# Optimization experiments

Measured on AMD Instinct MI355X. Metric: run time of the kernel, lower is better.

The kernel has to match this reference:

```python
import jax, jax.numpy as jnp
import numpy as np

N = 1024  # batch rows; each row has 480 features

def setup_inputs() -> dict:
    key = jax.random.key(0)
    kx, kS, kT, kH, kL = jax.random.split(key, 5)
    x = jax.random.normal(kx, (N, 480), dtype=jnp.float32)
    S = jax.random.normal(kS, (30, 2, 15), dtype=jnp.float32)    # buffer
    T = jax.random.normal(kT, (30, 15), dtype=jnp.float32)       # param
    H = jax.random.normal(kH, (45, 4096), dtype=jnp.float32)     # buffer (hash matrix)
    LUT = jax.random.normal(kL, (10, 4096, 2), dtype=jnp.float32)  # param (codebook)
    return {"x": x, "S": S, "T": T, "H": H, "LUT": LUT}

def reference(x, S, T, H, LUT):
    # (N, 480) -> (N, 8, 30, 2)
    x4 = x.reshape(-1, 8, 30, 2)
    # project each 2-vector through S: (N, 8, 30, 15)
    y = jnp.einsum('abcd,cdk->abck', x4, S) - T - 1e-4
    # straight-through sign-tanh binarization
    tanh = jnp.tanh(y)
    y = jax.lax.stop_gradient(jnp.sign(y) - tanh) + tanh
    # (N, 8, 10, 45): 30*15 = 10*(3*15)
    y = y.reshape(-1, 8, 10, 45)
    # hash scores over 4096 codes: (N, 8, 10, 4096)
    scores = jnp.einsum('bpcd,dk->bpck', y, H)
    idx = jnp.argmax(scores, axis=-1)  # (N, 8, 10) int
    # one_hot @ LUT is exactly a gather: out[b,p,c,:] = LUT[c, idx[b,p,c], :]
    out = LUT[jnp.arange(10)[None, None, :], idx]  # (N, 8, 10, 2)
    return out
```

## Files before the change

### kernel.cpp

```cpp
#include <hip/hip_runtime.h>
#include <math.h>

#define M_ROWS  81920
#define NCOLS   4096
#define KPAD    48
#define NCHUNK  4
#define CHUNKC  (NCOLS / NCHUNK)
#define CROUNDS (CHUNKC / 32)
#define GHALVES 3072
#define LO_SCALE 4096.0f
#define INV_LO   (1.0f / 4096.0f)

typedef _Float16 f16x8  __attribute__((ext_vector_type(8)));
typedef float    f32x16 __attribute__((ext_vector_type(16)));


__global__ void build_B_kernel(const float* __restrict__ H,
                               _Float16* __restrict__ Bfrag) {
    const int n = blockIdx.x * 256 + threadIdx.x;
    _Float16 hi[KPAD], lo[KPAD];
    #pragma unroll
    for (int k = 0; k < 45; ++k) {
        const float h = H[k * NCOLS + n];
        const _Float16 h1 = (_Float16)h;
        hi[k] = h1;
        lo[k] = (_Float16)((h - (float)h1) * LO_SCALE);
    }
    #pragma unroll
    for (int k = 45; k < KPAD; ++k) { hi[k] = (_Float16)0.f; lo[k] = (_Float16)0.f; }

    const int g = n >> 5;
    const int c = n & 31;
    _Float16* gbase = Bfrag + (size_t)g * GHALVES;
    #pragma unroll
    for (int f = 0; f < 6; ++f) {
        const int kt = (f < 3) ? f : f - 3;
        const _Float16* src = ((f < 3) ? hi : lo) + kt * 16;
        #pragma unroll
        for (int h = 0; h < 2; ++h) {
            *(f16x8*)(gbase + f * 512 + (h * 32 + c) * 8) =
                *(const f16x8*)(src + h * 8);
        }
    }
}

__global__ __launch_bounds__(512, 2) void score_argmax_kernel(
        const float* __restrict__ x,
        const float* __restrict__ S,
        const float* __restrict__ T,
        const _Float16* __restrict__ Bfrag,
        const float* __restrict__ LUT,
        float* __restrict__ out) {
    const int tid  = threadIdx.x;
    const int lane = tid & 63;
    const int l31  = lane & 31;
    const int half = lane >> 5;
    const int wid   = tid >> 6;
    const int chunk = wid & 3;
    const int rtile = wid >> 2;
    const int rowblk = blockIdx.x * 64;
    const int rowbase = rowblk + rtile * 32;

    __shared__ float lds_best[NCHUNK][64];
    __shared__ int   lds_bidx[NCHUNK][64];

    f16x8 afr[3];
    {
        const int row  = rowbase + l31;
        const int pair = row / 10;
        const int c2   = row - pair * 10;
        const int a    = pair >> 3;
        const int b    = pair & 7;
        const float* xp = x + a * 480 + b * 60;
        #pragma unroll
        for (int kt = 0; kt < 3; ++kt) {
            #pragma unroll
            for (int j = 0; j < 8; ++j) {
                const int k    = kt * 16 + half * 8 + j;
                const bool pad = (k >= 45);
                const int kcl  = pad ? 0 : k;
                const int cc   = kcl / 15;
                const int kk   = kcl - cc * 15;
                const int c    = c2 * 3 + cc;
                const float x0 = xp[c * 2 + 0];
                const float x1 = xp[c * 2 + 1];
                float v = x0 * S[(c * 2 + 0) * 15 + kk] + x1 * S[(c * 2 + 1) * 15 + kk];
                v = v - T[c * 15 + kk] - 1e-4f;
                const float yv = (v > 0.f) ? 1.f : ((v < 0.f) ? -1.f : 0.f);
                afr[kt][j] = pad ? (_Float16)0.f : (_Float16)yv;
            }
        }
    }

    float best[16];
    int   bidx[16];
    #pragma unroll
    for (int e = 0; e < 16; ++e) { best[e] = -INFINITY; bidx[e] = 0; }

    const int colbase0 = chunk * CHUNKC;
    const int gbase0   = colbase0 >> 5;
    const _Float16* lanep = Bfrag + (size_t)lane * 8;

#define PREFETCH(dst, rr) do {                                              \
        const _Float16* fp_ = lanep + (size_t)(gbase0 + (rr)) * GHALVES;    \
        _Pragma("unroll")                                                   \
        for (int f_ = 0; f_ < 6; ++f_)                                      \
            (dst)[f_] = *(const f16x8*)(fp_ + f_ * 512);                    \
    } while (0)

#define COMPUTE(buf, ct) do {                                               \
        f32x16 ch = {0.f};                                                  \
        f32x16 cl = {0.f};                                                  \
        ch = __builtin_amdgcn_mfma_f32_32x32x16_f16(afr[0], (buf)[0], ch, 0, 0, 0); \
        ch = __builtin_amdgcn_mfma_f32_32x32x16_f16(afr[1], (buf)[1], ch, 0, 0, 0); \
        ch = __builtin_amdgcn_mfma_f32_32x32x16_f16(afr[2], (buf)[2], ch, 0, 0, 0); \
        cl = __builtin_amdgcn_mfma_f32_32x32x16_f16(afr[0], (buf)[3], cl, 0, 0, 0); \
        cl = __builtin_amdgcn_mfma_f32_32x32x16_f16(afr[1], (buf)[4], cl, 0, 0, 0); \
        cl = __builtin_amdgcn_mfma_f32_32x32x16_f16(afr[2], (buf)[5], cl, 0, 0, 0); \
        const int mycol_ = colbase0 + (ct) * 32 + l31;                      \
        _Pragma("unroll")                                                   \
        for (int e_ = 0; e_ < 16; ++e_) {                                   \
            const float s_ = fmaf(cl[e_], INV_LO, ch[e_]);                  \
            if (s_ > best[e_]) bidx[e_] = mycol_;          \
            best[e_] = fmaxf(best[e_], s_);                                 \
        }                                                                   \
    } while (0)

    f16x8 cb[6], nb[6];
    PREFETCH(cb, 0);
    for (int it = 0; it < CROUNDS; it += 2) {
        PREFETCH(nb, it + 1);
        COMPUTE(cb, it);
        PREFETCH(cb, (it + 2) & 31);
        COMPUTE(nb, it + 1);
    }
#undef PREFETCH
#undef COMPUTE

    #pragma unroll
    for (int m = 1; m < 32; m <<= 1) {
        #pragma unroll
        for (int e = 0; e < 16; ++e) {
            const float ov = __shfl_xor(best[e], m, 64);
            const int   oi = __shfl_xor(bidx[e], m, 64);
            if (ov > best[e] || (ov == best[e] && oi < bidx[e])) {
                best[e] = ov; bidx[e] = oi;
            }
        }
    }

    if (l31 == 0) {
        #pragma unroll
        for (int e = 0; e < 16; ++e) {
            const int r64 = rtile * 32 + (e & 3) + 8 * (e >> 2) + 4 * half;
            lds_best[chunk][r64] = best[e];
            lds_bidx[chunk][r64] = bidx[e];
        }
    }
    __syncthreads();

    if (tid < 64) {
        const int row = rowblk + tid;
        float bv = lds_best[0][tid];
        int   bi = lds_bidx[0][tid];
        #pragma unroll
        for (int c = 1; c < NCHUNK; ++c) {
            const float v = lds_best[c][tid];
            const int   i = lds_bidx[c][tid];
            if (v > bv) { bv = v; bi = i; }
        }
        const int pair = row / 10;
        const int c2   = row - pair * 10;
        const float* l = LUT + ((size_t)c2 * NCOLS + bi) * 2;
        out[row * 2 + 0] = l[0];
        out[row * 2 + 1] = l[1];
    }
}

extern "C" void kernel_launch(void* const* d_in, const int* in_sizes, int n_in,
                              void* d_out, int out_size, void* d_ws, size_t ws_size,
                              hipStream_t stream) {
    const float* x   = (const float*)d_in[0];
    const float* S   = (const float*)d_in[1];
    const float* T   = (const float*)d_in[2];
    const float* H   = (const float*)d_in[3];
    const float* LUT = (const float*)d_in[4];
    float* out = (float*)d_out;

    _Float16* Bfrag = (_Float16*)d_ws;

    build_B_kernel<<<16, 256, 0, stream>>>(H, Bfrag);
    score_argmax_kernel<<<1280, 512, 0, stream>>>(x, S, T, Bfrag, LUT, out);
}
```

Before: 181.0 us.

## Split column chunks across blocks and merge argmax via 64-bit atomicMax

Each block now handles 256 rows for a single column chunk (8 waves, one row tile each) instead of 64 rows across 4 chunks. The cross-chunk argmax merge moves from a shared-memory reduction to a global atomicMax on a packed key (order-preserving float bits, inverted index for lowest-index ties), and a separate kernel then does the LUT gather. The intent is to drop the block-wide barrier and LDS step and to change how blocks share B-fragment loads. In exchange it adds global atomics, an extra kernel launch, and zeroing of the key buffer.

```diff
diff --git a/kernel.cpp b/kernel.cpp
--- a/kernel.cpp
+++ b/kernel.cpp
@@ -16,7 +16,8 @@
 
 
 __global__ void build_B_kernel(const float* __restrict__ H,
-                               _Float16* __restrict__ Bfrag) {
+                               _Float16* __restrict__ Bfrag,
+                               unsigned long long* __restrict__ keys) {
     const int n = blockIdx.x * 256 + threadIdx.x;
     _Float16 hi[KPAD], lo[KPAD];
     #pragma unroll
@@ -42,6 +43,8 @@
                 *(const f16x8*)(src + h * 8);
         }
     }
+    #pragma unroll
+    for (int i = 0; i < 20; ++i) keys[(size_t)n * 20 + i] = 0ull;
 }
 
 __global__ __launch_bounds__(512, 2) void score_argmax_kernel(
@@ -49,20 +52,15 @@
         const float* __restrict__ S,
         const float* __restrict__ T,
         const _Float16* __restrict__ Bfrag,
-        const float* __restrict__ LUT,
-        float* __restrict__ out) {
+        unsigned long long* __restrict__ keys) {
     const int tid  = threadIdx.x;
     const int lane = tid & 63;
     const int l31  = lane & 31;
     const int half = lane >> 5;
-    const int wid   = tid >> 6;
-    const int chunk = wid & 3;
-    const int rtile = wid >> 2;
-    const int rowblk = blockIdx.x * 64;
-    const int rowbase = rowblk + rtile * 32;
-
-    __shared__ float lds_best[NCHUNK][64];
-    __shared__ int   lds_bidx[NCHUNK][64];
+    const int wid  = tid >> 6;
+    const int chunk  = blockIdx.x / 320;
+    const int rowblk = (blockIdx.x - chunk * 320) * 256;
+    const int rowbase = rowblk + wid * 32;
 
     f16x8 afr[3];
     {
@@ -152,29 +150,28 @@
     if (l31 == 0) {
         #pragma unroll
         for (int e = 0; e < 16; ++e) {
-            const int r64 = rtile * 32 + (e & 3) + 8 * (e >> 2) + 4 * half;
-            lds_best[chunk][r64] = best[e];
-            lds_bidx[chunk][r64] = bidx[e];
+            const int row = rowbase + (e & 3) + 8 * (e >> 2) + 4 * half;
+            const unsigned u = __float_as_uint(best[e]);
+            const unsigned mono = (u & 0x80000000u) ? ~u : (u | 0x80000000u);
+            const unsigned long long key =
+                ((unsigned long long)mono << 32) | (unsigned)(4095 - bidx[e]);
+            atomicMax(&keys[row], key);
         }
     }
-    __syncthreads();
+}
 
-    if (tid < 64) {
-        const int row = rowblk + tid;
-        float bv = lds_best[0][tid];
-        int   bi = lds_bidx[0][tid];
-        #pragma unroll
-        for (int c = 1; c < NCHUNK; ++c) {
-            const float v = lds_best[c][tid];
-            const int   i = lds_bidx[c][tid];
-            if (v > bv) { bv = v; bi = i; }
-        }
-        const int pair = row / 10;
-        const int c2   = row - pair * 10;
-        const float* l = LUT + ((size_t)c2 * NCOLS + bi) * 2;
-        out[row * 2 + 0] = l[0];
-        out[row * 2 + 1] = l[1];
-    }
+__global__ void reduce_lut_kernel(const unsigned long long* __restrict__ keys,
+                                  const float* __restrict__ LUT,
+                                  float* __restrict__ out) {
+    const int row = blockIdx.x * blockDim.x + threadIdx.x;
+    if (row >= M_ROWS) return;
+    const unsigned long long key = keys[row];
+    const int bi = 4095 - (int)(key & 0xFFFFFFFFull);
+    const int pair = row / 10;
+    const int c2   = row - pair * 10;
+    const float* l = LUT + ((size_t)c2 * NCOLS + bi) * 2;
+    out[row * 2 + 0] = l[0];
+    out[row * 2 + 1] = l[1];
 }
 
 extern "C" void kernel_launch(void* const* d_in, const int* in_sizes, int n_in,
@@ -188,7 +185,10 @@
     float* out = (float*)d_out;
 
     _Float16* Bfrag = (_Float16*)d_ws;
+    unsigned long long* keys =
+        (unsigned long long*)(Bfrag + (size_t)128 * GHALVES);
 
-    build_B_kernel<<<16, 256, 0, stream>>>(H, Bfrag);
-    score_argmax_kernel<<<1280, 512, 0, stream>>>(x, S, T, Bfrag, LUT, out);
+    build_B_kernel<<<16, 256, 0, stream>>>(H, Bfrag, keys);
+    score_argmax_kernel<<<1280, 512, 0, stream>>>(x, S, T, Bfrag, keys);
+    reduce_lut_kernel<<<M_ROWS / 256, 256, 0, stream>>>(keys, LUT, out);
 }
```

After: 190.6 us. 5.3% more time.
